# Performance work log

Hardware: AMD Instinct MI355X
Metric: run time of the kernel (lower is better)

Reference implementation:

```python
import jax, jax.numpy as jnp
import numpy as np

N = 100000       # nodes
E = 1600000      # edges (avg degree 16)
C_IN = 128
C_OUT = 64
C_HID = 2 * C_OUT  # 128, matches GCNEncoder's 2*out_channels hidden width


def setup_inputs() -> dict:
    key = jax.random.key(0)
    k1, k2, k3, k4 = jax.random.split(key, 4)
    x = jax.random.normal(k1, (N, C_IN), dtype=jnp.float32)
    edge_index = jax.random.randint(k2, (2, E), 0, N, dtype=jnp.int64)
    # Glorot-ish scale for the linear weights (PyG GCNConv uses glorot init)
    W1 = jax.random.normal(k3, (C_IN, C_HID), dtype=jnp.float32) / np.sqrt(C_IN)
    b1 = jnp.zeros((C_HID,), dtype=jnp.float32)
    W2 = jax.random.normal(k4, (C_HID, C_OUT), dtype=jnp.float32) / np.sqrt(C_HID)
    b2 = jnp.zeros((C_OUT,), dtype=jnp.float32)
    return {"x": x, "edge_index": edge_index, "W1": W1, "b1": b1, "W2": W2, "b2": b2}


def _gcn_conv(x, src, dst, norm_e, self_norm, W, b):
    # GCNConv: out = D^{-1/2} (A + I) D^{-1/2} (x @ W) + b
    h = x @ W                                   # [N, C'] transform first (cheaper)
    msg = h[src] * norm_e[:, None]              # [E, C'] gather + edge normalization
    agg = jax.ops.segment_sum(msg, dst, num_segments=N)  # scatter-add over targets
    return agg + self_norm[:, None] * h + b     # self-loop term + bias


def reference(x, edge_index, W1, b1, W2, b2):
    src, dst = edge_index[0], edge_index[1]
    # degrees on A + I (self-loops added), identical for both layers
    deg = jax.ops.segment_sum(jnp.ones((E,), jnp.float32), dst, num_segments=N) + 1.0
    dinv = jax.lax.rsqrt(deg)                   # deg >= 1, no zero-guard needed
    norm_e = dinv[src] * dinv[dst]              # [E]
    self_norm = dinv * dinv                     # [N]

    h = _gcn_conv(x, src, dst, norm_e, self_norm, W1, b1)
    h = jax.nn.relu(h)
    return _gcn_conv(h, src, dst, norm_e, self_norm, W2, b2)
```

## Files before the change

kernel.cpp:

```cpp
#include <hip/hip_runtime.h>
#include <hip/hip_fp16.h>

#define NN   100000
#define NE   1600000
#define CIN  128
#define CHID 128
#define COUT 64

#define NPB  256
#define NB   391
#define NBLK 256
#define CHUNK ((NE + NBLK - 1) / NBLK)
#define BPAD 2048

typedef _Float16 f16x8 __attribute__((ext_vector_type(8)));
typedef float    f32x4 __attribute__((ext_vector_type(4)));

#define NTILE 782
#define GGRID 512

__global__ __launch_bounds__(512) void k_passA(const int* __restrict__ dst,
                                               int* __restrict__ tab) {
  __shared__ int hist[NB];
  int tid = threadIdx.x;
  for (int t = tid; t < NB; t += 512) hist[t] = 0;
  __syncthreads();
  int i0 = blockIdx.x * CHUNK;
  int i1 = min(i0 + CHUNK, NE);
  for (int i = i0 + tid; i < i1; i += 512)
    atomicAdd(&hist[((unsigned)dst[i]) >> 8], 1);
  __syncthreads();
  for (int t = tid; t < NB; t += 512)
    tab[t * NBLK + blockIdx.x] = hist[t];
}

__global__ __launch_bounds__(512) void k_scan(int* __restrict__ tab,
                                              int* __restrict__ bb) {
  __shared__ int s[512];
  int t = threadIdx.x;
  int v = 0;
  if (t < NB) {
    const int* row = tab + t * NBLK;
#pragma unroll 8
    for (int k = 0; k < NBLK; k++) v += row[k];
  }
  s[t] = v;
  __syncthreads();
  for (int off = 1; off < 512; off <<= 1) {
    int u = (t >= off) ? s[t - off] : 0;
    __syncthreads();
    s[t] += u;
    __syncthreads();
  }
  int base = s[t] - v;
  if (t < NB) bb[t] = base;
  if (t == 0) bb[NB] = NE;
  if (t < NB) {
    int run = base;
    int* row = tab + t * NBLK;
    for (int k = 0; k < NBLK; k += 4) {
      int4 c = *(int4*)(row + k);
      int4 w;
      w.x = run; run += c.x;
      w.y = run; run += c.y;
      w.z = run; run += c.z;
      w.w = run; run += c.w;
      *(int4*)(row + k) = w;
    }
  }
}

__global__ __launch_bounds__(256, 2) void k_pbg1(const int* __restrict__ src,
                                                 const int* __restrict__ dst,
                                                 const int* __restrict__ tab,
                                                 int* __restrict__ barr,
                                                 const float* __restrict__ X,
                                                 const float* __restrict__ W,
                                                 __half* __restrict__ G) {
  __shared__ _Float16 Wt[128][128];
  __shared__ int cur[NB];
  int tid = threadIdx.x;
  int bid = blockIdx.x;

  if (bid < NBLK) {
    for (int t = tid; t < NB; t += 256) cur[t] = tab[t * NBLK + bid];
    __syncthreads();
    int i0 = bid * CHUNK;
    int i1 = min(i0 + CHUNK, NE);
    for (int i = i0 + tid; i < i1; i += 256) {
      int d = dst[i];
      unsigned b = ((unsigned)d) >> 8;
      int p = atomicAdd(&cur[b], 1);
      barr[p] = (src[i] << 8) | (d & 255);
    }
    return;
  }

  for (int i = tid; i < 128 * 32; i += 256) {
    int k = i >> 5, c4 = (i & 31) << 2;
    float4 v = ((const float4*)W)[i];
    Wt[c4 + 0][k] = (_Float16)v.x;
    Wt[c4 + 1][k] = (_Float16)v.y;
    Wt[c4 + 2][k] = (_Float16)v.z;
    Wt[c4 + 3][k] = (_Float16)v.w;
  }
  __syncthreads();
  int wv = tid >> 6, lane = tid & 63;
  int l15 = lane & 15, g = lane >> 4;

  f16x8 wf[8][4];
#pragma unroll
  for (int cf = 0; cf < 8; cf++)
#pragma unroll
    for (int ks = 0; ks < 4; ks++)
      wf[cf][ks] = *(const f16x8*)&Wt[cf * 16 + l15][ks * 32 + g * 8];

  for (int t = bid - NBLK; t < NTILE; t += GGRID) {
    int rowbase = t * 128 + wv * 32;
    f32x4 acc[2][8];
#pragma unroll
    for (int i = 0; i < 2; i++)
#pragma unroll
      for (int j = 0; j < 8; j++) acc[i][j] = (f32x4){0.f, 0.f, 0.f, 0.f};

    int r0 = min(rowbase + l15, NN - 1);
    int r1 = min(rowbase + 16 + l15, NN - 1);
    const float* p0 = X + (size_t)r0 * CIN + g * 8;
    const float* p1 = X + (size_t)r1 * CIN + g * 8;

    float4 u0a = *(const float4*)p0, u0b = *(const float4*)(p0 + 4);
    float4 u1a = *(const float4*)p1, u1b = *(const float4*)(p1 + 4);

#pragma unroll
    for (int ks = 0; ks < 4; ks++) {
      f16x8 xa, xb;
      xa[0] = (_Float16)u0a.x; xa[1] = (_Float16)u0a.y;
      xa[2] = (_Float16)u0a.z; xa[3] = (_Float16)u0a.w;
      xa[4] = (_Float16)u0b.x; xa[5] = (_Float16)u0b.y;
      xa[6] = (_Float16)u0b.z; xa[7] = (_Float16)u0b.w;
      xb[0] = (_Float16)u1a.x; xb[1] = (_Float16)u1a.y;
      xb[2] = (_Float16)u1a.z; xb[3] = (_Float16)u1a.w;
      xb[4] = (_Float16)u1b.x; xb[5] = (_Float16)u1b.y;
      xb[6] = (_Float16)u1b.z; xb[7] = (_Float16)u1b.w;
      if (ks < 3) {
        int o = (ks + 1) * 32;
        u0a = *(const float4*)(p0 + o); u0b = *(const float4*)(p0 + o + 4);
        u1a = *(const float4*)(p1 + o); u1b = *(const float4*)(p1 + o + 4);
      }
#pragma unroll
      for (int cf = 0; cf < 8; cf++) {
        acc[0][cf] = __builtin_amdgcn_mfma_f32_16x16x32_f16(wf[cf][ks], xa, acc[0][cf], 0, 0, 0);
        acc[1][cf] = __builtin_amdgcn_mfma_f32_16x16x32_f16(wf[cf][ks], xb, acc[1][cf], 0, 0, 0);
      }
    }

#pragma unroll
    for (int rf = 0; rf < 2; rf++) {
      int row = rowbase + rf * 16 + l15;
      if (row < NN) {
#pragma unroll
        for (int cf = 0; cf < 8; cf++) {
          int col = cf * 16 + g * 4;
          __half2 h0 = __half2(__float2half(acc[rf][cf][0]),
                               __float2half(acc[rf][cf][1]));
          __half2 h1 = __half2(__float2half(acc[rf][cf][2]),
                               __float2half(acc[rf][cf][3]));
          uint2 s;
          s.x = *(unsigned*)&h0;
          s.y = *(unsigned*)&h1;
          *(uint2*)(G + (size_t)row * CHID + col) = s;
        }
      }
    }
  }
}

__global__ __launch_bounds__(256) void k_l2(const int* __restrict__ barr,
                                            const int* __restrict__ bb,
                                            int* __restrict__ csr,
                                            int* __restrict__ rs,
                                            int* __restrict__ re,
                                            float* __restrict__ dinv,
                                            __half* __restrict__ g1,
                                            __half* __restrict__ g2) {
  __shared__ int lcnt[NPB];
  __shared__ int lcur[NPB];
  int b = blockIdx.x, t = threadIdx.x;
  if (b == 0) {
    if (t < 128) g1[(size_t)NN * CHID + t] = __float2half(0.f);
    if (t < 64)  g2[(size_t)NN * COUT + t] = __float2half(0.f);
    if (t == 0)  dinv[NN] = 0.f;
  }
  int e0 = bb[b], e1 = bb[b + 1];
  lcnt[t] = 0;
  __syncthreads();
  for (int i = e0 + t; i < e1; i += 256) atomicAdd(&lcnt[barr[i] & 255], 1);
  __syncthreads();
  int v = lcnt[t];
  int pv = (v + 7) & ~7;
  lcur[t] = pv;
  __syncthreads();
  for (int off = 1; off < 256; off <<= 1) {
    int u = (t >= off) ? lcur[t - off] : 0;
    __syncthreads();
    lcur[t] += u;
    __syncthreads();
  }
  int pex = lcur[t] - pv;
  int start = e0 + b * BPAD + pex;
  int g = b * NPB + t;
  if (g < NN) {
    rs[g] = start;
    re[g] = start + pv;
    dinv[g] = rsqrtf((float)v + 1.0f);
  }
  __syncthreads();
  lcur[t] = start;
  for (int k = v; k < pv; k++) csr[start + k] = NN;
  __syncthreads();
  for (int i = e0 + t; i < e1; i += 256) {
    int w = barr[i];
    int p = atomicAdd(&lcur[w & 255], 1);
    csr[p] = ((unsigned)w) >> 8;
  }
}

__global__ __launch_bounds__(256, 2) void k_gemm2(const __half* __restrict__ X,
                                                  const float* __restrict__ W,
                                                  const float* __restrict__ dinv,
                                                  __half* __restrict__ G) {
  __shared__ _Float16 Wt[64][128];
  int tid = threadIdx.x;
  for (int i = tid; i < 128 * 16; i += 256) {
    int k = i >> 4, c4 = (i & 15) << 2;
    float4 v = ((const float4*)W)[i];
    Wt[c4 + 0][k] = (_Float16)v.x;
    Wt[c4 + 1][k] = (_Float16)v.y;
    Wt[c4 + 2][k] = (_Float16)v.z;
    Wt[c4 + 3][k] = (_Float16)v.w;
  }
  __syncthreads();
  int wv = tid >> 6, lane = tid & 63;
  int l15 = lane & 15, g = lane >> 4;

  f16x8 wf[4][4];
#pragma unroll
  for (int cf = 0; cf < 4; cf++)
#pragma unroll
    for (int ks = 0; ks < 4; ks++)
      wf[cf][ks] = *(const f16x8*)&Wt[cf * 16 + l15][ks * 32 + g * 8];

  for (int t = blockIdx.x; t < NTILE; t += GGRID) {
    int rowbase = t * 128 + wv * 32;
    f32x4 acc[2][4];
#pragma unroll
    for (int i = 0; i < 2; i++)
#pragma unroll
      for (int j = 0; j < 4; j++) acc[i][j] = (f32x4){0.f, 0.f, 0.f, 0.f};

    int r0 = min(rowbase + l15, NN - 1);
    int r1 = min(rowbase + 16 + l15, NN - 1);
    const _Float16* p0 = (const _Float16*)X + (size_t)r0 * CHID + g * 8;
    const _Float16* p1 = (const _Float16*)X + (size_t)r1 * CHID + g * 8;

    f16x8 xa = *(const f16x8*)p0;
    f16x8 xb = *(const f16x8*)p1;

#pragma unroll
    for (int ks = 0; ks < 4; ks++) {
      f16x8 ca = xa, cb = xb;
      if (ks < 3) {
        int o = (ks + 1) * 32;
        xa = *(const f16x8*)(p0 + o);
        xb = *(const f16x8*)(p1 + o);
      }
#pragma unroll
      for (int cf = 0; cf < 4; cf++) {
        acc[0][cf] = __builtin_amdgcn_mfma_f32_16x16x32_f16(wf[cf][ks], ca, acc[0][cf], 0, 0, 0);
        acc[1][cf] = __builtin_amdgcn_mfma_f32_16x16x32_f16(wf[cf][ks], cb, acc[1][cf], 0, 0, 0);
      }
    }

#pragma unroll
    for (int rf = 0; rf < 2; rf++) {
      int row = rowbase + rf * 16 + l15;
      if (row < NN) {
        float dn = dinv[row];
#pragma unroll
        for (int cf = 0; cf < 4; cf++) {
          int col = cf * 16 + g * 4;
          __half2 h0 = __half2(__float2half(dn * acc[rf][cf][0]),
                               __float2half(dn * acc[rf][cf][1]));
          __half2 h1 = __half2(__float2half(dn * acc[rf][cf][2]),
                               __float2half(dn * acc[rf][cf][3]));
          uint2 s;
          s.x = *(unsigned*)&h0;
          s.y = *(unsigned*)&h1;
          *(uint2*)(G + (size_t)row * COUT + col) = s;
        }
      }
    }
  }
}

#define ACC8F(A, V, D)                                                        \
  {                                                                           \
    float2 f;                                                                 \
    f = __half22float2(*(__half2*)&(V).x); A[0] = fmaf(D, f.x, A[0]); A[1] = fmaf(D, f.y, A[1]); \
    f = __half22float2(*(__half2*)&(V).y); A[2] = fmaf(D, f.x, A[2]); A[3] = fmaf(D, f.y, A[3]); \
    f = __half22float2(*(__half2*)&(V).z); A[4] = fmaf(D, f.x, A[4]); A[5] = fmaf(D, f.y, A[5]); \
    f = __half22float2(*(__half2*)&(V).w); A[6] = fmaf(D, f.x, A[6]); A[7] = fmaf(D, f.y, A[7]); \
  }

#define ACC8(A, V)                                                  \
  {                                                                 \
    float2 f;                                                       \
    f = __half22float2(*(__half2*)&(V).x); A[0] += f.x; A[1] += f.y; \
    f = __half22float2(*(__half2*)&(V).y); A[2] += f.x; A[3] += f.y; \
    f = __half22float2(*(__half2*)&(V).z); A[4] += f.x; A[5] += f.y; \
    f = __half22float2(*(__half2*)&(V).w); A[6] += f.x; A[7] += f.y; \
  }

__global__ __launch_bounds__(256) void k_agg1(const __half* __restrict__ g,
                                              const int* __restrict__ rs,
                                              const int* __restrict__ re,
                                              const float* __restrict__ dinv,
                                              const int* __restrict__ csr,
                                              const float* __restrict__ b,
                                              __half* __restrict__ o) {
  int wid = (blockIdx.x * blockDim.x + threadIdx.x) >> 6;
  int lane = threadIdx.x & 63;
  if (wid >= NN) return;
  int q = lane >> 4, ql = lane & 15;
  const uint4* gp = (const uint4*)g;

  float aA[8] = {0.f, 0.f, 0.f, 0.f, 0.f, 0.f, 0.f, 0.f};
  float aB[8] = {0.f, 0.f, 0.f, 0.f, 0.f, 0.f, 0.f, 0.f};

  float dnw = dinv[wid];
  if (q == 0) {
    uint4 v = gp[(size_t)wid * 16 + ql];
    ACC8F(aA, v, dnw);
  }

  int i0 = rs[wid], i1 = re[wid];
  for (int i = i0; i < i1; i += 8) {
    int sA = csr[i + q];
    int sB = csr[i + 4 + q];
    float dA = dinv[sA];
    float dB = dinv[sB];
    uint4 vA = gp[(size_t)sA * 16 + ql];
    uint4 vB = gp[(size_t)sB * 16 + ql];
    ACC8F(aA, vA, dA);
    ACC8F(aB, vB, dB);
  }

  float r[8];
#pragma unroll
  for (int c = 0; c < 8; c++) {
    float t = aA[c] + aB[c];
    t += __shfl_xor(t, 16);
    t += __shfl_xor(t, 32);
    r[c] = t;
  }
  if (q == 0) {
    float4 b0 = *(const float4*)(b + 8 * ql);
    float4 b1 = *(const float4*)(b + 8 * ql + 4);
    __half2 h[4];
    h[0] = __half2(__float2half(fmaxf(fmaf(dnw, r[0], b0.x), 0.f)),
                   __float2half(fmaxf(fmaf(dnw, r[1], b0.y), 0.f)));
    h[1] = __half2(__float2half(fmaxf(fmaf(dnw, r[2], b0.z), 0.f)),
                   __float2half(fmaxf(fmaf(dnw, r[3], b0.w), 0.f)));
    h[2] = __half2(__float2half(fmaxf(fmaf(dnw, r[4], b1.x), 0.f)),
                   __float2half(fmaxf(fmaf(dnw, r[5], b1.y), 0.f)));
    h[3] = __half2(__float2half(fmaxf(fmaf(dnw, r[6], b1.z), 0.f)),
                   __float2half(fmaxf(fmaf(dnw, r[7], b1.w), 0.f)));
    *(uint4*)(o + (size_t)wid * CHID + 8 * ql) = *(uint4*)h;
  }
}

__global__ __launch_bounds__(256) void k_agg2(const __half* __restrict__ g,
                                              const int* __restrict__ rs,
                                              const int* __restrict__ re,
                                              const float* __restrict__ dinv,
                                              const int* __restrict__ csr,
                                              const float* __restrict__ b,
                                              float* __restrict__ o) {
  int wid = (blockIdx.x * blockDim.x + threadIdx.x) >> 6;
  int lane = threadIdx.x & 63;
  if (wid >= NN) return;
  int g8 = lane >> 3, gl = lane & 7;
  const uint4* gp = (const uint4*)g;

  float aA[8] = {0.f, 0.f, 0.f, 0.f, 0.f, 0.f, 0.f, 0.f};

  if (g8 == 0) {
    uint4 v = gp[(size_t)wid * 8 + gl];
    ACC8(aA, v);
  }

  int i0 = rs[wid], i1 = re[wid];
  for (int i = i0; i < i1; i += 8) {
    int s = csr[i + g8];
    uint4 v = gp[(size_t)s * 8 + gl];
    ACC8(aA, v);
  }

  float r[8];
#pragma unroll
  for (int c = 0; c < 8; c++) {
    float t = aA[c];
    t += __shfl_xor(t, 8);
    t += __shfl_xor(t, 16);
    t += __shfl_xor(t, 32);
    r[c] = t;
  }
  if (g8 == 0) {
    float dn = dinv[wid];
    float4 b0 = *(const float4*)(b + 8 * gl);
    float4 b1 = *(const float4*)(b + 8 * gl + 4);
    float4 o0 = make_float4(fmaf(dn, r[0], b0.x), fmaf(dn, r[1], b0.y),
                            fmaf(dn, r[2], b0.z), fmaf(dn, r[3], b0.w));
    float4 o1v = make_float4(fmaf(dn, r[4], b1.x), fmaf(dn, r[5], b1.y),
                             fmaf(dn, r[6], b1.z), fmaf(dn, r[7], b1.w));
    *(float4*)(o + (size_t)wid * COUT + 8 * gl) = o0;
    *(float4*)(o + (size_t)wid * COUT + 8 * gl + 4) = o1v;
  }
}


extern "C" void kernel_launch(void* const* d_in, const int* in_sizes, int n_in,
                              void* d_out, int out_size, void* d_ws, size_t ws_size,
                              hipStream_t stream) {
  const float* x  = (const float*)d_in[0];
  const int*   ei = (const int*)d_in[1];
  const float* W1 = (const float*)d_in[2];
  const float* b1 = (const float*)d_in[3];
  const float* W2 = (const float*)d_in[4];
  const float* b2 = (const float*)d_in[5];
  float* out = (float*)d_out;

  const int* esrc = ei;
  const int* edst = ei + NE;

  char* p = (char*)d_ws;
  __half* g1 = (__half*)p;    p += (size_t)(NN + 1) * CHID * 2;
  __half* o1 = (__half*)p;    p += (size_t)NN * CHID * 2;
  __half* g2 = (__half*)p;    p += (size_t)(NN + 1) * COUT * 2;
  int* rs  = (int*)p;         p += (size_t)NN * 4;
  int* re  = (int*)p;         p += (size_t)NN * 4;
  float* dinv = (float*)p;    p += (size_t)(NN + 1) * 4;
  int* tab = (int*)p;         p += (size_t)NB * NBLK * 4;
  int* bb  = (int*)p;         p += (size_t)(NB + 1) * 4;
  int* barr = (int*)p;        p += (size_t)NE * 4;
  int* csr = (int*)p;         p += (size_t)(NE + NB * BPAD) * 4;

  hipLaunchKernelGGL(k_passA, dim3(NBLK), dim3(512), 0, stream, edst, tab);
  hipLaunchKernelGGL(k_scan, dim3(1), dim3(512), 0, stream, tab, bb);
  hipLaunchKernelGGL(k_pbg1, dim3(NBLK + GGRID), dim3(256), 0, stream,
                     esrc, edst, tab, barr, x, W1, g1);
  hipLaunchKernelGGL(k_l2, dim3(NB), dim3(256), 0, stream, barr, bb, csr, rs, re,
                     dinv, g1, g2);

  hipLaunchKernelGGL(k_agg1, dim3((NN + 3) / 4), dim3(256), 0, stream,
                     g1, rs, re, dinv, csr, b1, o1);

  hipLaunchKernelGGL(k_gemm2, dim3(GGRID), dim3(256), 0, stream, o1, W2, dinv, g2);
  hipLaunchKernelGGL(k_agg2, dim3((NN + 3) / 4), dim3(256), 0, stream,
                     g2, rs, re, dinv, csr, b2, out);
}
```

Baseline: 248.9 us.

## Move layer-1 GEMM into histogram pass and split binning into its own kernel

```diff
diff --git a/kernel.cpp b/kernel.cpp
--- a/kernel.cpp
+++ b/kernel.cpp
@@ -9,7 +9,7 @@
 
 #define NPB  256
 #define NB   391
-#define NBLK 256
+#define NBLK 128
 #define CHUNK ((NE + NBLK - 1) / NBLK)
 #define BPAD 2048
 
@@ -18,20 +18,90 @@
 
 #define NTILE 782
 #define GGRID 512
-
-__global__ __launch_bounds__(512) void k_passA(const int* __restrict__ dst,
-                                               int* __restrict__ tab) {
+#define G1B   384
+
+__global__ __launch_bounds__(512) void k_pag1(const int* __restrict__ dst,
+                                              int* __restrict__ tab,
+                                              const float* __restrict__ X,
+                                              const float* __restrict__ W,
+                                              __half* __restrict__ G) {
   __shared__ int hist[NB];
+  __shared__ _Float16 Wt[128][128];
   int tid = threadIdx.x;
-  for (int t = tid; t < NB; t += 512) hist[t] = 0;
-  __syncthreads();
-  int i0 = blockIdx.x * CHUNK;
-  int i1 = min(i0 + CHUNK, NE);
-  for (int i = i0 + tid; i < i1; i += 512)
-    atomicAdd(&hist[((unsigned)dst[i]) >> 8], 1);
-  __syncthreads();
-  for (int t = tid; t < NB; t += 512)
-    tab[t * NBLK + blockIdx.x] = hist[t];
+  int bid = blockIdx.x;
+
+  if (bid < NBLK) {
+    for (int t = tid; t < NB; t += 512) hist[t] = 0;
+    __syncthreads();
+    int i0 = bid * CHUNK;
+    int i1 = min(i0 + CHUNK, NE);
+    for (int i = i0 + tid; i < i1; i += 512)
+      atomicAdd(&hist[((unsigned)dst[i]) >> 8], 1);
+    __syncthreads();
+    for (int t = tid; t < NB; t += 512)
+      tab[t * NBLK + bid] = hist[t];
+    return;
+  }
+
+  for (int i = tid; i < 128 * 32; i += 512) {
+    int k = i >> 5, c4 = (i & 31) << 2;
+    float4 v = ((const float4*)W)[i];
+    Wt[c4 + 0][k] = (_Float16)v.x;
+    Wt[c4 + 1][k] = (_Float16)v.y;
+    Wt[c4 + 2][k] = (_Float16)v.z;
+    Wt[c4 + 3][k] = (_Float16)v.w;
+  }
+  __syncthreads();
+  int wv = tid >> 6, lane = tid & 63;
+  int l15 = lane & 15, g = lane >> 4;
+
+  f16x8 wf[8][4];
+#pragma unroll
+  for (int cf = 0; cf < 8; cf++)
+#pragma unroll
+    for (int ks = 0; ks < 4; ks++)
+      wf[cf][ks] = *(const f16x8*)&Wt[cf * 16 + l15][ks * 32 + g * 8];
+
+  for (int t = bid - NBLK; t < NTILE; t += G1B) {
+    int rowbase = t * 128 + wv * 16;
+    f32x4 acc[8];
+#pragma unroll
+    for (int j = 0; j < 8; j++) acc[j] = (f32x4){0.f, 0.f, 0.f, 0.f};
+
+    int r0 = min(rowbase + l15, NN - 1);
+    const float* p0 = X + (size_t)r0 * CIN + g * 8;
+    float4 u0a = *(const float4*)p0, u0b = *(const float4*)(p0 + 4);
+
+#pragma unroll
+    for (int ks = 0; ks < 4; ks++) {
+      f16x8 xa;
+      xa[0] = (_Float16)u0a.x; xa[1] = (_Float16)u0a.y;
+      xa[2] = (_Float16)u0a.z; xa[3] = (_Float16)u0a.w;
+      xa[4] = (_Float16)u0b.x; xa[5] = (_Float16)u0b.y;
+      xa[6] = (_Float16)u0b.z; xa[7] = (_Float16)u0b.w;
+      if (ks < 3) {
+        int o = (ks + 1) * 32;
+        u0a = *(const float4*)(p0 + o); u0b = *(const float4*)(p0 + o + 4);
+      }
+#pragma unroll
+      for (int cf = 0; cf < 8; cf++)
+        acc[cf] = __builtin_amdgcn_mfma_f32_16x16x32_f16(wf[cf][ks], xa, acc[cf], 0, 0, 0);
+    }
+
+    int row = rowbase + l15;
+    if (row < NN) {
+#pragma unroll
+      for (int cf = 0; cf < 8; cf++) {
+        int col = cf * 16 + g * 4;
+        __half2 h0 = __half2(__float2half(acc[cf][0]), __float2half(acc[cf][1]));
+        __half2 h1 = __half2(__float2half(acc[cf][2]), __float2half(acc[cf][3]));
+        uint2 s;
+        s.x = *(unsigned*)&h0;
+        s.y = *(unsigned*)&h1;
+        *(uint2*)(G + (size_t)row * CHID + col) = s;
+      }
+    }
+  }
 }
 
 __global__ __launch_bounds__(512) void k_scan(int* __restrict__ tab,
@@ -70,108 +140,21 @@
   }
 }
 
-__global__ __launch_bounds__(256, 2) void k_pbg1(const int* __restrict__ src,
-                                                 const int* __restrict__ dst,
-                                                 const int* __restrict__ tab,
-                                                 int* __restrict__ barr,
-                                                 const float* __restrict__ X,
-                                                 const float* __restrict__ W,
-                                                 __half* __restrict__ G) {
-  __shared__ _Float16 Wt[128][128];
+__global__ __launch_bounds__(512) void k_passB(const int* __restrict__ src,
+                                               const int* __restrict__ dst,
+                                               const int* __restrict__ tab,
+                                               int* __restrict__ barr) {
   __shared__ int cur[NB];
   int tid = threadIdx.x;
-  int bid = blockIdx.x;
-
-  if (bid < NBLK) {
-    for (int t = tid; t < NB; t += 256) cur[t] = tab[t * NBLK + bid];
-    __syncthreads();
-    int i0 = bid * CHUNK;
-    int i1 = min(i0 + CHUNK, NE);
-    for (int i = i0 + tid; i < i1; i += 256) {
-      int d = dst[i];
-      unsigned b = ((unsigned)d) >> 8;
-      int p = atomicAdd(&cur[b], 1);
-      barr[p] = (src[i] << 8) | (d & 255);
-    }
-    return;
-  }
-
-  for (int i = tid; i < 128 * 32; i += 256) {
-    int k = i >> 5, c4 = (i & 31) << 2;
-    float4 v = ((const float4*)W)[i];
-    Wt[c4 + 0][k] = (_Float16)v.x;
-    Wt[c4 + 1][k] = (_Float16)v.y;
-    Wt[c4 + 2][k] = (_Float16)v.z;
-    Wt[c4 + 3][k] = (_Float16)v.w;
-  }
-  __syncthreads();
-  int wv = tid >> 6, lane = tid & 63;
-  int l15 = lane & 15, g = lane >> 4;
-
-  f16x8 wf[8][4];
-#pragma unroll
-  for (int cf = 0; cf < 8; cf++)
-#pragma unroll
-    for (int ks = 0; ks < 4; ks++)
-      wf[cf][ks] = *(const f16x8*)&Wt[cf * 16 + l15][ks * 32 + g * 8];
-
-  for (int t = bid - NBLK; t < NTILE; t += GGRID) {
-    int rowbase = t * 128 + wv * 32;
-    f32x4 acc[2][8];
-#pragma unroll
-    for (int i = 0; i < 2; i++)
-#pragma unroll
-      for (int j = 0; j < 8; j++) acc[i][j] = (f32x4){0.f, 0.f, 0.f, 0.f};
-
-    int r0 = min(rowbase + l15, NN - 1);
-    int r1 = min(rowbase + 16 + l15, NN - 1);
-    const float* p0 = X + (size_t)r0 * CIN + g * 8;
-    const float* p1 = X + (size_t)r1 * CIN + g * 8;
-
-    float4 u0a = *(const float4*)p0, u0b = *(const float4*)(p0 + 4);
-    float4 u1a = *(const float4*)p1, u1b = *(const float4*)(p1 + 4);
-
-#pragma unroll
-    for (int ks = 0; ks < 4; ks++) {
-      f16x8 xa, xb;
-      xa[0] = (_Float16)u0a.x; xa[1] = (_Float16)u0a.y;
-      xa[2] = (_Float16)u0a.z; xa[3] = (_Float16)u0a.w;
-      xa[4] = (_Float16)u0b.x; xa[5] = (_Float16)u0b.y;
-      xa[6] = (_Float16)u0b.z; xa[7] = (_Float16)u0b.w;
-      xb[0] = (_Float16)u1a.x; xb[1] = (_Float16)u1a.y;
-      xb[2] = (_Float16)u1a.z; xb[3] = (_Float16)u1a.w;
-      xb[4] = (_Float16)u1b.x; xb[5] = (_Float16)u1b.y;
-      xb[6] = (_Float16)u1b.z; xb[7] = (_Float16)u1b.w;
-      if (ks < 3) {
-        int o = (ks + 1) * 32;
-        u0a = *(const float4*)(p0 + o); u0b = *(const float4*)(p0 + o + 4);
-        u1a = *(const float4*)(p1 + o); u1b = *(const float4*)(p1 + o + 4);
-      }
-#pragma unroll
-      for (int cf = 0; cf < 8; cf++) {
-        acc[0][cf] = __builtin_amdgcn_mfma_f32_16x16x32_f16(wf[cf][ks], xa, acc[0][cf], 0, 0, 0);
-        acc[1][cf] = __builtin_amdgcn_mfma_f32_16x16x32_f16(wf[cf][ks], xb, acc[1][cf], 0, 0, 0);
-      }
-    }
-
-#pragma unroll
-    for (int rf = 0; rf < 2; rf++) {
-      int row = rowbase + rf * 16 + l15;
-      if (row < NN) {
-#pragma unroll
-        for (int cf = 0; cf < 8; cf++) {
-          int col = cf * 16 + g * 4;
-          __half2 h0 = __half2(__float2half(acc[rf][cf][0]),
-                               __float2half(acc[rf][cf][1]));
-          __half2 h1 = __half2(__float2half(acc[rf][cf][2]),
-                               __float2half(acc[rf][cf][3]));
-          uint2 s;
-          s.x = *(unsigned*)&h0;
-          s.y = *(unsigned*)&h1;
-          *(uint2*)(G + (size_t)row * CHID + col) = s;
-        }
-      }
-    }
+  for (int t = tid; t < NB; t += 512) cur[t] = tab[t * NBLK + blockIdx.x];
+  __syncthreads();
+  int i0 = blockIdx.x * CHUNK;
+  int i1 = min(i0 + CHUNK, NE);
+  for (int i = i0 + tid; i < i1; i += 512) {
+    int d = dst[i];
+    unsigned b = ((unsigned)d) >> 8;
+    int p = atomicAdd(&cur[b], 1);
+    barr[p] = (src[i] << 8) | (d & 255);
   }
 }
 
@@ -303,6 +286,15 @@
   }
 }
 
+#define ACC8(A, V)                                                  \
+  {                                                                 \
+    float2 f;                                                       \
+    f = __half22float2(*(__half2*)&(V).x); A[0] += f.x; A[1] += f.y; \
+    f = __half22float2(*(__half2*)&(V).y); A[2] += f.x; A[3] += f.y; \
+    f = __half22float2(*(__half2*)&(V).z); A[4] += f.x; A[5] += f.y; \
+    f = __half22float2(*(__half2*)&(V).w); A[6] += f.x; A[7] += f.y; \
+  }
+
 #define ACC8F(A, V, D)                                                        \
   {                                                                           \
     float2 f;                                                                 \
@@ -310,15 +302,6 @@
     f = __half22float2(*(__half2*)&(V).y); A[2] = fmaf(D, f.x, A[2]); A[3] = fmaf(D, f.y, A[3]); \
     f = __half22float2(*(__half2*)&(V).z); A[4] = fmaf(D, f.x, A[4]); A[5] = fmaf(D, f.y, A[5]); \
     f = __half22float2(*(__half2*)&(V).w); A[6] = fmaf(D, f.x, A[6]); A[7] = fmaf(D, f.y, A[7]); \
-  }
-
-#define ACC8(A, V)                                                  \
-  {                                                                 \
-    float2 f;                                                       \
-    f = __half22float2(*(__half2*)&(V).x); A[0] += f.x; A[1] += f.y; \
-    f = __half22float2(*(__half2*)&(V).y); A[2] += f.x; A[3] += f.y; \
-    f = __half22float2(*(__half2*)&(V).z); A[4] += f.x; A[5] += f.y; \
-    f = __half22float2(*(__half2*)&(V).w); A[6] += f.x; A[7] += f.y; \
   }
 
 __global__ __launch_bounds__(256) void k_agg1(const __half* __restrict__ g,
@@ -455,10 +438,10 @@
   int* barr = (int*)p;        p += (size_t)NE * 4;
   int* csr = (int*)p;         p += (size_t)(NE + NB * BPAD) * 4;
 
-  hipLaunchKernelGGL(k_passA, dim3(NBLK), dim3(512), 0, stream, edst, tab);
+  hipLaunchKernelGGL(k_pag1, dim3(NBLK + G1B), dim3(512), 0, stream,
+                     edst, tab, x, W1, g1);
   hipLaunchKernelGGL(k_scan, dim3(1), dim3(512), 0, stream, tab, bb);
-  hipLaunchKernelGGL(k_pbg1, dim3(NBLK + GGRID), dim3(256), 0, stream,
-                     esrc, edst, tab, barr, x, W1, g1);
+  hipLaunchKernelGGL(k_passB, dim3(NBLK), dim3(512), 0, stream, esrc, edst, tab, barr);
   hipLaunchKernelGGL(k_l2, dim3(NB), dim3(256), 0, stream, barr, bb, csr, rs, re,
                      dinv, g1, g2);
 
```

Result: faster. 233.7 us (-6.1%).
